# Optimization experiments

Hardware: AMD Instinct MI355X
Metric: run time of the kernel (lower is better)

## Reference

```python
import jax, jax.numpy as jnp
import numpy as np

B, T, I, H, SEQLEN = 16384, 60, 32, 128, 30


def setup_inputs() -> dict:
    key = jax.random.key(0)
    ks = jax.random.split(key, 8)
    s_ih = 1.0 / np.sqrt(H)
    return {
        "x": jax.random.normal(ks[0], (B, T, I), dtype=jnp.float32),
        "h": jax.random.normal(ks[1], (1, B, H), dtype=jnp.float32),
        # GRU params (PyTorch layout: gates [r, z, n] stacked along dim 0)
        "W_ih": jax.random.uniform(ks[2], (3 * H, I), minval=-s_ih, maxval=s_ih, dtype=jnp.float32),
        "W_hh": jax.random.uniform(ks[3], (3 * H, H), minval=-s_ih, maxval=s_ih, dtype=jnp.float32),
        "b_ih": jax.random.uniform(ks[4], (3 * H,), minval=-s_ih, maxval=s_ih, dtype=jnp.float32),
        "b_hh": jax.random.uniform(ks[5], (3 * H,), minval=-s_ih, maxval=s_ih, dtype=jnp.float32),
        # output projection: hidden -> n_inputs
        "W_out": jax.random.uniform(ks[6], (I, H), minval=-s_ih, maxval=s_ih, dtype=jnp.float32),
        "b_out": jax.random.uniform(ks[7], (I,), minval=-s_ih, maxval=s_ih, dtype=jnp.float32),
    }


def _gru_cell(x_t, h, W_ih, W_hh, b_ih, b_hh):
    # x_t: [B, I], h: [B, H]
    gi = x_t @ W_ih.T + b_ih          # [B, 3H]
    gh = h @ W_hh.T + b_hh            # [B, 3H]
    i_r, i_z, i_n = jnp.split(gi, 3, axis=-1)
    h_r, h_z, h_n = jnp.split(gh, 3, axis=-1)
    r = jax.nn.sigmoid(i_r + h_r)
    z = jax.nn.sigmoid(i_z + h_z)
    n = jnp.tanh(i_n + r * h_n)
    return (1.0 - z) * n + z * h


def reference(x, h, W_ih, W_hh, b_ih, b_hh, W_out, b_out):
    xout = x[:, SEQLEN:, :]            # [B, steps, I]
    steps = xout.shape[1]
    h0 = h[0]                          # single layer, unidirectional -> [B, H]
    x0 = xout[:, 0, :]                 # [B, I]

    def step(carry, _):
        x_t, h_t = carry
        h_new = _gru_cell(x_t, h_t, W_ih, W_hh, b_ih, b_hh)
        y = h_new @ W_out.T + b_out    # [B, I], fed back as next input
        return (y, h_new), y

    _, ys = jax.lax.scan(step, (x0, h0), None, length=steps)  # ys: [steps, B, I]
    return jnp.transpose(ys, (1, 0, 2))                        # [B, steps, I]
```

## Files before the change

kernel.cpp:

```cpp
#include <hip/hip_runtime.h>


#define NB    16384
#define TT    60
#define II    32
#define HH    128
#define NSTEP 30
#define SEQ0  30
#define BM    64
#define XBS   40
#define ROWB  256
#define BUFB  (BM * ROWB)

#define WS_WSTAR 0
#define WS_BSTAR (384 * 128)

#define S_RZ (-1.4426950408889634f)
#define S_N  ( 2.8853900817779268f)

typedef __attribute__((ext_vector_type(8))) short bf16x8;
typedef __attribute__((ext_vector_type(4))) float f32x4;

#define MFMA(a, b, c) __builtin_amdgcn_mfma_f32_16x16x32_bf16((a), (b), (c), 0, 0, 0)

#define LDS_BARRIER() do {                                          \
    asm volatile("s_waitcnt lgkmcnt(0)\n\ts_barrier" ::: "memory"); \
    __builtin_amdgcn_sched_barrier(0);                              \
} while (0)

#define EXP2(x) __builtin_amdgcn_exp2f(x)
#define RCP(x)  __builtin_amdgcn_rcpf(x)

__device__ __forceinline__ short f2bf(float x) {
    unsigned u = __float_as_uint(x);
    u += 0x7FFFu + ((u >> 16) & 1u);
    return (short)(u >> 16);
}
__device__ __forceinline__ unsigned cvt_pk_bf16(float lo, float hi) {
    unsigned r;
    asm("v_cvt_pk_bf16_f32 %0, %1, %2" : "=v"(r) : "v"(lo), "v"(hi));
    return r;
}
__device__ __forceinline__ bf16x8 ldw8(const float* p) {
    float4 a = *(const float4*)p;
    float4 b = *(const float4*)(p + 4);
    bf16x8 f;
    f[0] = f2bf(a.x); f[1] = f2bf(a.y); f[2] = f2bf(a.z); f[3] = f2bf(a.w);
    f[4] = f2bf(b.x); f[5] = f2bf(b.y); f[6] = f2bf(b.z); f[7] = f2bf(b.w);
    return f;
}
__device__ __forceinline__ bf16x8 ldw8s(const float* p, float s) {
    float4 a = *(const float4*)p;
    float4 b = *(const float4*)(p + 4);
    bf16x8 f;
    f[0] = f2bf(a.x * s); f[1] = f2bf(a.y * s); f[2] = f2bf(a.z * s); f[3] = f2bf(a.w * s);
    f[4] = f2bf(b.x * s); f[5] = f2bf(b.y * s); f[6] = f2bf(b.z * s); f[7] = f2bf(b.w * s);
    return f;
}
__device__ __forceinline__ float sigm2(float ap) { return RCP(1.0f + EXP2(ap)); }
__device__ __forceinline__ float tanh2(float tp) {
    return fmaf(-2.0f, RCP(1.0f + EXP2(tp)), 1.0f);
}

__global__ void fold_kernel(const float* __restrict__ Wih,
                            const float* __restrict__ Whh,
                            const float* __restrict__ bih,
                            const float* __restrict__ bhh,
                            const float* __restrict__ Wout,
                            const float* __restrict__ bout,
                            float* __restrict__ ws)
{
    const int jg = blockIdx.x;
    const int k  = threadIdx.x;
    const int gate = jg >> 7;
    const float sc = (gate < 2) ? S_RZ : S_N;
    float acc  = (gate < 2) ? Whh[(size_t)jg * HH + k] : 0.0f;
    float bacc = 0.0f;
    #pragma unroll 8
    for (int i = 0; i < II; ++i) {
        const float w = Wih[(size_t)jg * II + i];
        acc  += w * Wout[(size_t)i * HH + k];
        bacc += w * bout[i];
    }
    ws[WS_WSTAR + (size_t)jg * HH + k] = acc * sc;
    if (k == 0)
        ws[WS_BSTAR + jg] = (bih[jg] + ((gate < 2) ? bhh[jg] : 0.0f) + bacc) * sc;
}

__global__ __launch_bounds__(512, 1)
void gru_mfma_kernel(const float* __restrict__ x,
                     const float* __restrict__ h0,
                     const float* __restrict__ Wih,
                     const float* __restrict__ Whh,
                     const float* __restrict__ bih,
                     const float* __restrict__ bhh,
                     const float* __restrict__ Wout,
                     const float* __restrict__ bout,
                     const float* __restrict__ ws,
                     float* __restrict__ out)
{
    __shared__ short shb[2][BM * 128];
    __shared__ short sxb[BM * XBS];
    char* shbb = (char*)shb;

    const int tid    = threadIdx.x;
    const int lane   = tid & 63;
    const int wave   = __builtin_amdgcn_readfirstlane(tid >> 6);
    const int n16    = lane & 15;
    const int quad   = lane >> 4;
    const int rowblk = blockIdx.x * BM;
    const int j      = wave * 16 + n16;

    int rb[4];
    #pragma unroll
    for (int kt = 0; kt < 4; ++kt)
        rb[kt] = n16 * 256 + ((kt * 64 + quad * 16) ^ (n16 << 4));
    int wb[4];
    #pragma unroll
    for (int rg = 0; rg < 4; ++rg)
        wb[rg] = quad * 1024 + ((2 * j) ^ (quad << 6) ^ (rg << 4));

    bf16x8 Bnh[4];
    float  b_nh;
    {
        const float* wn = Whh + (size_t)(2 * HH + j) * HH;
        #pragma unroll
        for (int kt = 0; kt < 4; ++kt)
            Bnh[kt] = ldw8s(wn + kt * 32 + quad * 8, S_N);
        b_nh = bhh[2 * HH + j] * S_N;
    }
    const int rowtile = wave >> 1;
    const int coltile = wave & 1;
    bf16x8 Bo[4];
    float  b_o;
    {
        const int i = coltile * 16 + n16;
        #pragma unroll
        for (int kt = 0; kt < 4; ++kt)
            Bo[kt] = ldw8(Wout + (size_t)i * HH + kt * 32 + quad * 8);
        b_o = bout[i];
    }

    float hst[4][4];
    #pragma unroll
    for (int mt = 0; mt < 4; ++mt)
        #pragma unroll
        for (int reg = 0; reg < 4; ++reg)
            hst[mt][reg] = h0[(size_t)(rowblk + mt * 16 + quad * 4 + reg) * HH + j];

    float* yp0;
    float* yp1;
    {
        const int r0 = rowblk + rowtile * 16 + quad * 4;
        yp0 = out + (size_t)r0 * (NSTEP * II) + coltile * 16 + n16;
        yp1 = yp0 + 2 * (size_t)(NSTEP * II);
    }

    {
        const int r  = tid >> 3;
        const int cb = (tid & 7) * 32;
        const int sw = (r & 15) << 4;
        const float* src = h0 + (size_t)(rowblk + r) * HH + (tid & 7) * 16;
        *(bf16x8*)(shbb + r * ROWB + (cb ^ sw))        = ldw8(src);
        *(bf16x8*)(shbb + r * ROWB + ((cb + 16) ^ sw)) = ldw8(src + 8);
    }
    if (tid < 256) {
        const int r  = tid >> 2;
        const int c0 = (tid & 3) * 8;
        *(bf16x8*)&sxb[r * XBS + c0] = ldw8(x + ((size_t)(rowblk + r) * TT + SEQ0) * II + c0);
    }
    __syncthreads();

    {
        bf16x8 Br0[4], Bz0[4], Bxr, Bxz, Bxn;
        const float* wr = Whh + (size_t)j * HH;
        const float* wz = Whh + (size_t)(HH + j) * HH;
        #pragma unroll
        for (int kt = 0; kt < 4; ++kt) {
            Br0[kt] = ldw8s(wr + kt * 32 + quad * 8, S_RZ);
            Bz0[kt] = ldw8s(wz + kt * 32 + quad * 8, S_RZ);
        }
        Bxr = ldw8s(Wih + (size_t)j * II + quad * 8, S_RZ);
        Bxz = ldw8s(Wih + (size_t)(HH + j) * II + quad * 8, S_RZ);
        Bxn = ldw8s(Wih + (size_t)(2 * HH + j) * II + quad * 8, S_N);
        const float b_r0 = (bih[j] + bhh[j]) * S_RZ;
        const float b_z0 = (bih[HH + j] + bhh[HH + j]) * S_RZ;
        const float b_n0 = bih[2 * HH + j] * S_N;

        #pragma unroll
        for (int mt = 0; mt < 4; ++mt) {
            f32x4 ar  = (f32x4){b_r0, b_r0, b_r0, b_r0};
            f32x4 az  = (f32x4){b_z0, b_z0, b_z0, b_z0};
            f32x4 anh = (f32x4){b_nh, b_nh, b_nh, b_nh};
            f32x4 anx = (f32x4){b_n0, b_n0, b_n0, b_n0};
            #pragma unroll
            for (int kt = 0; kt < 4; ++kt) {
                bf16x8 A = *(const bf16x8*)(shbb + rb[kt] + mt * 4096);
                ar  = MFMA(A, Br0[kt], ar);
                az  = MFMA(A, Bz0[kt], az);
                anh = MFMA(A, Bnh[kt], anh);
            }
            {
                bf16x8 Ax = *(const bf16x8*)&sxb[(mt * 16 + n16) * XBS + quad * 8];
                ar  = MFMA(Ax, Bxr, ar);
                az  = MFMA(Ax, Bxz, az);
                anx = MFMA(Ax, Bxn, anx);
            }
            float hn[4];
            #pragma unroll
            for (int reg = 0; reg < 4; ++reg) {
                const float r = sigm2(ar[reg]);
                const float z = sigm2(az[reg]);
                const float n = tanh2(anx[reg] + r * anh[reg]);
                const float hnew = n + z * (hst[mt][reg] - n);
                hst[mt][reg] = hnew;
                hn[reg] = hnew;
            }
            const unsigned pk01 = cvt_pk_bf16(hn[0], hn[1]);
            const unsigned pk23 = cvt_pk_bf16(hn[2], hn[3]);
            *(short*)(shbb + BUFB + wb[0] + mt * 4096)       = (short)pk01;
            *(short*)(shbb + BUFB + wb[1] + mt * 4096 + 256) = (short)(pk01 >> 16);
            *(short*)(shbb + BUFB + wb[2] + mt * 4096 + 512) = (short)pk23;
            *(short*)(shbb + BUFB + wb[3] + mt * 4096 + 768) = (short)(pk23 >> 16);
        }
    }

    bf16x8 Brs[4], Bzs[4], Bni[4];
    float  b_rs, b_zs, b_ni;
    {
        const float* pr = ws + WS_WSTAR + (size_t)j * HH;
        const float* pz = ws + WS_WSTAR + (size_t)(HH + j) * HH;
        const float* pn = ws + WS_WSTAR + (size_t)(2 * HH + j) * HH;
        #pragma unroll
        for (int kt = 0; kt < 4; ++kt) {
            Brs[kt] = ldw8(pr + kt * 32 + quad * 8);
            Bzs[kt] = ldw8(pz + kt * 32 + quad * 8);
            Bni[kt] = ldw8(pn + kt * 32 + quad * 8);
        }
        b_rs = ws[WS_BSTAR + j];
        b_zs = ws[WS_BSTAR + HH + j];
        b_ni = ws[WS_BSTAR + 2 * HH + j];
    }

    __syncthreads();

    auto body = [&](int s, int qb, bool last) {
        (void)s;
        const int rdoff = qb * BUFB;
        {
            f32x4 yo = (f32x4){b_o, b_o, b_o, b_o};
            #pragma unroll
            for (int kt = 0; kt < 4; ++kt) {
                bf16x8 A2 = *(const bf16x8*)(shbb + rdoff + rb[kt] + rowtile * 4096);
                yo = MFMA(A2, Bo[kt], yo);
            }
            yp0[0]         = yo[0];
            yp0[NSTEP*II]  = yo[1];
            yp1[0]         = yo[2];
            yp1[NSTEP*II]  = yo[3];
            yp0 += II;
            yp1 += II;
        }
        if (last) return;

        const int wroff = (qb ^ 1) * BUFB;
        #pragma unroll
        for (int mt = 0; mt < 4; ++mt) {
            f32x4 ar  = (f32x4){b_rs, b_rs, b_rs, b_rs};
            f32x4 az  = (f32x4){b_zs, b_zs, b_zs, b_zs};
            f32x4 anh = (f32x4){b_nh, b_nh, b_nh, b_nh};
            f32x4 ani = (f32x4){b_ni, b_ni, b_ni, b_ni};
            #pragma unroll
            for (int kt = 0; kt < 4; ++kt) {
                bf16x8 A = *(const bf16x8*)(shbb + rdoff + rb[kt] + mt * 4096);
                ar  = MFMA(A, Brs[kt], ar);
                az  = MFMA(A, Bzs[kt], az);
                anh = MFMA(A, Bnh[kt], anh);
                ani = MFMA(A, Bni[kt], ani);
            }
            float hn[4];
            #pragma unroll
            for (int reg = 0; reg < 4; ++reg) {
                const float r = sigm2(ar[reg]);
                const float z = sigm2(az[reg]);
                const float n = tanh2(ani[reg] + r * anh[reg]);
                const float hnew = n + z * (hst[mt][reg] - n);
                hst[mt][reg] = hnew;
                hn[reg] = hnew;
            }
            const unsigned pk01 = cvt_pk_bf16(hn[0], hn[1]);
            const unsigned pk23 = cvt_pk_bf16(hn[2], hn[3]);
            *(short*)(shbb + wroff + wb[0] + mt * 4096)       = (short)pk01;
            *(short*)(shbb + wroff + wb[1] + mt * 4096 + 256) = (short)(pk01 >> 16);
            *(short*)(shbb + wroff + wb[2] + mt * 4096 + 512) = (short)pk23;
            *(short*)(shbb + wroff + wb[3] + mt * 4096 + 768) = (short)(pk23 >> 16);
        }
        LDS_BARRIER();
    };

    for (int s2 = 0; s2 < NSTEP - 2; s2 += 2) {
        body(s2,     1, false);
        body(s2 + 1, 0, false);
    }
    body(NSTEP - 2, 1, false);
    body(NSTEP - 1, 0, true);
}

extern "C" void kernel_launch(void* const* d_in, const int* in_sizes, int n_in,
                              void* d_out, int out_size, void* d_ws, size_t ws_size,
                              hipStream_t stream) {
    (void)in_sizes; (void)n_in; (void)out_size; (void)ws_size;
    const float* x    = (const float*)d_in[0];
    const float* h0   = (const float*)d_in[1];
    const float* Wih  = (const float*)d_in[2];
    const float* Whh  = (const float*)d_in[3];
    const float* bih  = (const float*)d_in[4];
    const float* bhh  = (const float*)d_in[5];
    const float* Wout = (const float*)d_in[6];
    const float* bout = (const float*)d_in[7];
    float* out = (float*)d_out;
    float* ws  = (float*)d_ws;

    fold_kernel<<<dim3(384), dim3(128), 0, stream>>>(Wih, Whh, bih, bhh,
                                                     Wout, bout, ws);
    dim3 grid(NB / BM);
    dim3 block(512);
    gru_mfma_kernel<<<grid, block, 0, stream>>>(x, h0, Wih, Whh, bih, bhh,
                                                Wout, bout, ws, out);
}
```

Baseline: 256.8 us.

## Split each 64-row block across 16 waves and stage W_out in LDS

Doubles the block to 1024 threads so each column-tile wave handles only half of the 64 rows, with two row-halves each covering 32 rows. This halves per-wave MFMA and gate work per step and the number of hidden-state registers held. The output projection weights move from per-wave registers into shared memory, and only the first 8 waves compute the output projection. The aim is more wave-level parallelism per CU to hide MFMA and transcendental latency in the serial recurrence. The cost is larger barriers, extra LDS reads for W_out, and uneven work between waves.

```diff
diff --git a/kernel.cpp b/kernel.cpp
--- a/kernel.cpp
+++ b/kernel.cpp
@@ -87,7 +87,7 @@
         ws[WS_BSTAR + jg] = (bih[jg] + ((gate < 2) ? bhh[jg] : 0.0f) + bacc) * sc;
 }
 
-__global__ __launch_bounds__(512, 1)
+__global__ __launch_bounds__(1024, 1)
 void gru_mfma_kernel(const float* __restrict__ x,
                      const float* __restrict__ h0,
                      const float* __restrict__ Wih,
@@ -101,6 +101,7 @@
 {
     __shared__ short shb[2][BM * 128];
     __shared__ short sxb[BM * XBS];
+    __shared__ short sWo[2 * 4 * 64 * 8];
     char* shbb = (char*)shb;
 
     const int tid    = threadIdx.x;
@@ -109,16 +110,24 @@
     const int n16    = lane & 15;
     const int quad   = lane >> 4;
     const int rowblk = blockIdx.x * BM;
-    const int j      = wave * 16 + n16;
+    const int ct     = wave & 7;
+    const int rh     = wave >> 3;
+    const int j      = ct * 16 + n16;
 
     int rb[4];
     #pragma unroll
     for (int kt = 0; kt < 4; ++kt)
-        rb[kt] = n16 * 256 + ((kt * 64 + quad * 16) ^ (n16 << 4));
+        rb[kt] = rh * 8192 + n16 * 256 + ((kt * 64 + quad * 16) ^ (n16 << 4));
     int wb[4];
     #pragma unroll
     for (int rg = 0; rg < 4; ++rg)
-        wb[rg] = quad * 1024 + ((2 * j) ^ (quad << 6) ^ (rg << 4));
+        wb[rg] = rh * 8192 + quad * 1024 + ((2 * j) ^ (quad << 6) ^ (rg << 4));
+    const int rowtile = (wave >> 1) & 3;
+    const int coltile = wave & 1;
+    int rb2[4];
+    #pragma unroll
+    for (int kt = 0; kt < 4; ++kt)
+        rb2[kt] = rowtile * 4096 + n16 * 256 + ((kt * 64 + quad * 16) ^ (n16 << 4));
 
     bf16x8 Bnh[4];
     float  b_nh;
@@ -129,24 +138,22 @@
             Bnh[kt] = ldw8s(wn + kt * 32 + quad * 8, S_N);
         b_nh = bhh[2 * HH + j] * S_N;
     }
-    const int rowtile = wave >> 1;
-    const int coltile = wave & 1;
-    bf16x8 Bo[4];
-    float  b_o;
-    {
-        const int i = coltile * 16 + n16;
-        #pragma unroll
-        for (int kt = 0; kt < 4; ++kt)
-            Bo[kt] = ldw8(Wout + (size_t)i * HH + kt * 32 + quad * 8);
-        b_o = bout[i];
-    }
-
-    float hst[4][4];
+    if (wave < 2) {
+        #pragma unroll
+        for (int kt = 0; kt < 4; ++kt) {
+            bf16x8 t = ldw8(Wout + (size_t)(wave * 16 + n16) * HH + kt * 32 + quad * 8);
+            *(bf16x8*)&sWo[((wave * 4 + kt) * 64 + lane) * 8] = t;
+        }
+    }
+    const float b_o = bout[coltile * 16 + n16];
+
+    float hst[2][4];
     #pragma unroll
-    for (int mt = 0; mt < 4; ++mt)
+    for (int mt = 0; mt < 2; ++mt)
         #pragma unroll
         for (int reg = 0; reg < 4; ++reg)
-            hst[mt][reg] = h0[(size_t)(rowblk + mt * 16 + quad * 4 + reg) * HH + j];
+            hst[mt][reg] =
+                h0[(size_t)(rowblk + rh * 32 + mt * 16 + quad * 4 + reg) * HH + j];
 
     float* yp0;
     float* yp1;
@@ -157,12 +164,11 @@
     }
 
     {
-        const int r  = tid >> 3;
-        const int cb = (tid & 7) * 32;
+        const int r  = tid >> 4;
+        const int cb = (tid & 15) * 16;
         const int sw = (r & 15) << 4;
-        const float* src = h0 + (size_t)(rowblk + r) * HH + (tid & 7) * 16;
-        *(bf16x8*)(shbb + r * ROWB + (cb ^ sw))        = ldw8(src);
-        *(bf16x8*)(shbb + r * ROWB + ((cb + 16) ^ sw)) = ldw8(src + 8);
+        *(bf16x8*)(shbb + r * ROWB + (cb ^ sw)) =
+            ldw8(h0 + (size_t)(rowblk + r) * HH + (tid & 15) * 8);
     }
     if (tid < 256) {
         const int r  = tid >> 2;
@@ -188,7 +194,7 @@
         const float b_n0 = bih[2 * HH + j] * S_N;
 
         #pragma unroll
-        for (int mt = 0; mt < 4; ++mt) {
+        for (int mt = 0; mt < 2; ++mt) {
             f32x4 ar  = (f32x4){b_r0, b_r0, b_r0, b_r0};
             f32x4 az  = (f32x4){b_z0, b_z0, b_z0, b_z0};
             f32x4 anh = (f32x4){b_nh, b_nh, b_nh, b_nh};
@@ -201,7 +207,7 @@
                 anh = MFMA(A, Bnh[kt], anh);
             }
             {
-                bf16x8 Ax = *(const bf16x8*)&sxb[(mt * 16 + n16) * XBS + quad * 8];
+                bf16x8 Ax = *(const bf16x8*)&sxb[(rh * 32 + mt * 16 + n16) * XBS + quad * 8];
                 ar  = MFMA(Ax, Bxr, ar);
                 az  = MFMA(Ax, Bxz, az);
                 anx = MFMA(Ax, Bxn, anx);
@@ -244,20 +250,20 @@
 
     __syncthreads();
 
-    auto body = [&](int s, int qb, bool last) {
-        (void)s;
+    auto body = [&](int qb, bool last) {
         const int rdoff = qb * BUFB;
-        {
+        if (wave < 8) {
             f32x4 yo = (f32x4){b_o, b_o, b_o, b_o};
             #pragma unroll
             for (int kt = 0; kt < 4; ++kt) {
-                bf16x8 A2 = *(const bf16x8*)(shbb + rdoff + rb[kt] + rowtile * 4096);
-                yo = MFMA(A2, Bo[kt], yo);
-            }
-            yp0[0]         = yo[0];
-            yp0[NSTEP*II]  = yo[1];
-            yp1[0]         = yo[2];
-            yp1[NSTEP*II]  = yo[3];
+                bf16x8 A2  = *(const bf16x8*)(shbb + rdoff + rb2[kt]);
+                bf16x8 Bof = *(const bf16x8*)&sWo[((coltile * 4 + kt) * 64 + lane) * 8];
+                yo = MFMA(A2, Bof, yo);
+            }
+            yp0[0]        = yo[0];
+            yp0[NSTEP*II] = yo[1];
+            yp1[0]        = yo[2];
+            yp1[NSTEP*II] = yo[3];
             yp0 += II;
             yp1 += II;
         }
@@ -265,7 +271,7 @@
 
         const int wroff = (qb ^ 1) * BUFB;
         #pragma unroll
-        for (int mt = 0; mt < 4; ++mt) {
+        for (int mt = 0; mt < 2; ++mt) {
             f32x4 ar  = (f32x4){b_rs, b_rs, b_rs, b_rs};
             f32x4 az  = (f32x4){b_zs, b_zs, b_zs, b_zs};
             f32x4 anh = (f32x4){b_nh, b_nh, b_nh, b_nh};
@@ -299,11 +305,11 @@
     };
 
     for (int s2 = 0; s2 < NSTEP - 2; s2 += 2) {
-        body(s2,     1, false);
-        body(s2 + 1, 0, false);
-    }
-    body(NSTEP - 2, 1, false);
-    body(NSTEP - 1, 0, true);
+        body(1, false);
+        body(0, false);
+    }
+    body(1, false);
+    body(0, true);
 }
 
 extern "C" void kernel_launch(void* const* d_in, const int* in_sizes, int n_in,
@@ -324,7 +330,7 @@
     fold_kernel<<<dim3(384), dim3(128), 0, stream>>>(Wih, Whh, bih, bhh,
                                                      Wout, bout, ws);
     dim3 grid(NB / BM);
-    dim3 block(512);
+    dim3 block(1024);
     gru_mfma_kernel<<<grid, block, 0, stream>>>(x, h0, Wih, Whh, bih, bhh,
                                                 Wout, bout, ws, out);
 }
```

After: 274.4 us. 1.07x slower.

## Software-pipeline GRU step so gate MFMAs overlap activations of previous tile

Applied to the files above, without the earlier changes.

Restructures each recurrent step so MFMA work for row tiles runs one or two tiles ahead of the sigmoid/tanh activation and LDS writeback of earlier tiles, with sched_barriers fixing the interleave. The output-projection global stores are also deferred until after some gate MFMAs are issued, so their latency is hidden. Bias vectors are hoisted into preformed f32x4 registers. This raises register pressure from holding up to three tiles of accumulators at once, which could cause spills at 512 threads.

```diff
diff --git a/kernel.cpp b/kernel.cpp
--- a/kernel.cpp
+++ b/kernel.cpp
@@ -27,6 +27,8 @@
     asm volatile("s_waitcnt lgkmcnt(0)\n\ts_barrier" ::: "memory"); \
     __builtin_amdgcn_sched_barrier(0);                              \
 } while (0)
+
+#define SB() __builtin_amdgcn_sched_barrier(0)
 
 #define EXP2(x) __builtin_amdgcn_exp2f(x)
 #define RCP(x)  __builtin_amdgcn_rcpf(x)
@@ -86,6 +88,40 @@
     if (k == 0)
         ws[WS_BSTAR + jg] = (bih[jg] + ((gate < 2) ? bhh[jg] : 0.0f) + bacc) * sc;
 }
+
+#define MT_MFMA(mt, ar, az, anh, ani, rdoff) do {                              \
+    bf16x8 A0_ = *(const bf16x8*)(shbb + (rdoff) + rb[0] + (mt) * 4096);       \
+    bf16x8 A1_ = *(const bf16x8*)(shbb + (rdoff) + rb[1] + (mt) * 4096);       \
+    bf16x8 A2_ = *(const bf16x8*)(shbb + (rdoff) + rb[2] + (mt) * 4096);       \
+    bf16x8 A3_ = *(const bf16x8*)(shbb + (rdoff) + rb[3] + (mt) * 4096);       \
+    ar  = MFMA(A0_, Brs[0], vb_r);  az  = MFMA(A0_, Bzs[0], vb_z);             \
+    anh = MFMA(A0_, Bnh[0], vb_nh); ani = MFMA(A0_, Bni[0], vb_ni);            \
+    ar  = MFMA(A1_, Brs[1], ar);    az  = MFMA(A1_, Bzs[1], az);               \
+    anh = MFMA(A1_, Bnh[1], anh);   ani = MFMA(A1_, Bni[1], ani);              \
+    ar  = MFMA(A2_, Brs[2], ar);    az  = MFMA(A2_, Bzs[2], az);               \
+    anh = MFMA(A2_, Bnh[2], anh);   ani = MFMA(A2_, Bni[2], ani);              \
+    ar  = MFMA(A3_, Brs[3], ar);    az  = MFMA(A3_, Bzs[3], az);               \
+    anh = MFMA(A3_, Bnh[3], anh);   ani = MFMA(A3_, Bni[3], ani);              \
+} while (0)
+
+#define ACT_MT(mt, ar, az, anh, ani, wroff) do {                               \
+    float hn_[4];                                                              \
+    _Pragma("unroll")                                                          \
+    for (int rg_ = 0; rg_ < 4; ++rg_) {                                        \
+        const float r_ = sigm2((ar)[rg_]);                                     \
+        const float z_ = sigm2((az)[rg_]);                                     \
+        const float n_ = tanh2((ani)[rg_] + r_ * (anh)[rg_]);                  \
+        const float h_ = n_ + z_ * (hst[mt][rg_] - n_);                        \
+        hst[mt][rg_] = h_;                                                     \
+        hn_[rg_] = h_;                                                         \
+    }                                                                          \
+    const unsigned pkA_ = cvt_pk_bf16(hn_[0], hn_[1]);                         \
+    const unsigned pkB_ = cvt_pk_bf16(hn_[2], hn_[3]);                         \
+    *(short*)(shbb + (wroff) + wb[0] + (mt) * 4096)       = (short)pkA_;       \
+    *(short*)(shbb + (wroff) + wb[1] + (mt) * 4096 + 256) = (short)(pkA_ >> 16); \
+    *(short*)(shbb + (wroff) + wb[2] + (mt) * 4096 + 512) = (short)pkB_;       \
+    *(short*)(shbb + (wroff) + wb[3] + (mt) * 4096 + 768) = (short)(pkB_ >> 16); \
+} while (0)
 
 __global__ __launch_bounds__(512, 1)
 void gru_mfma_kernel(const float* __restrict__ x,
@@ -226,7 +262,7 @@
     }
 
     bf16x8 Brs[4], Bzs[4], Bni[4];
-    float  b_rs, b_zs, b_ni;
+    f32x4  vb_r, vb_z, vb_nh, vb_ni, vb_o;
     {
         const float* pr = ws + WS_WSTAR + (size_t)j * HH;
         const float* pz = ws + WS_WSTAR + (size_t)(HH + j) * HH;
@@ -237,73 +273,73 @@
             Bzs[kt] = ldw8(pz + kt * 32 + quad * 8);
             Bni[kt] = ldw8(pn + kt * 32 + quad * 8);
         }
-        b_rs = ws[WS_BSTAR + j];
-        b_zs = ws[WS_BSTAR + HH + j];
-        b_ni = ws[WS_BSTAR + 2 * HH + j];
+        const float b_rs = ws[WS_BSTAR + j];
+        const float b_zs = ws[WS_BSTAR + HH + j];
+        const float b_ni = ws[WS_BSTAR + 2 * HH + j];
+        vb_r  = (f32x4){b_rs, b_rs, b_rs, b_rs};
+        vb_z  = (f32x4){b_zs, b_zs, b_zs, b_zs};
+        vb_nh = (f32x4){b_nh, b_nh, b_nh, b_nh};
+        vb_ni = (f32x4){b_ni, b_ni, b_ni, b_ni};
+        vb_o  = (f32x4){b_o,  b_o,  b_o,  b_o};
     }
 
     __syncthreads();
 
-    auto body = [&](int s, int qb, bool last) {
-        (void)s;
+    auto body = [&](int qb, bool last) {
         const int rdoff = qb * BUFB;
+        f32x4 yo;
         {
-            f32x4 yo = (f32x4){b_o, b_o, b_o, b_o};
-            #pragma unroll
-            for (int kt = 0; kt < 4; ++kt) {
-                bf16x8 A2 = *(const bf16x8*)(shbb + rdoff + rb[kt] + rowtile * 4096);
-                yo = MFMA(A2, Bo[kt], yo);
-            }
-            yp0[0]         = yo[0];
-            yp0[NSTEP*II]  = yo[1];
-            yp1[0]         = yo[2];
-            yp1[NSTEP*II]  = yo[3];
-            yp0 += II;
-            yp1 += II;
-        }
-        if (last) return;
-
+            bf16x8 Y0 = *(const bf16x8*)(shbb + rdoff + rb[0] + rowtile * 4096);
+            bf16x8 Y1 = *(const bf16x8*)(shbb + rdoff + rb[1] + rowtile * 4096);
+            bf16x8 Y2 = *(const bf16x8*)(shbb + rdoff + rb[2] + rowtile * 4096);
+            bf16x8 Y3 = *(const bf16x8*)(shbb + rdoff + rb[3] + rowtile * 4096);
+            yo = MFMA(Y0, Bo[0], vb_o);
+            yo = MFMA(Y1, Bo[1], yo);
+            yo = MFMA(Y2, Bo[2], yo);
+            yo = MFMA(Y3, Bo[3], yo);
+        }
+        if (last) {
+            yp0[0]        = yo[0];
+            yp0[NSTEP*II] = yo[1];
+            yp1[0]        = yo[2];
+            yp1[NSTEP*II] = yo[3];
+            return;
+        }
         const int wroff = (qb ^ 1) * BUFB;
-        #pragma unroll
-        for (int mt = 0; mt < 4; ++mt) {
-            f32x4 ar  = (f32x4){b_rs, b_rs, b_rs, b_rs};
-            f32x4 az  = (f32x4){b_zs, b_zs, b_zs, b_zs};
-            f32x4 anh = (f32x4){b_nh, b_nh, b_nh, b_nh};
-            f32x4 ani = (f32x4){b_ni, b_ni, b_ni, b_ni};
-            #pragma unroll
-            for (int kt = 0; kt < 4; ++kt) {
-                bf16x8 A = *(const bf16x8*)(shbb + rdoff + rb[kt] + mt * 4096);
-                ar  = MFMA(A, Brs[kt], ar);
-                az  = MFMA(A, Bzs[kt], az);
-                anh = MFMA(A, Bnh[kt], anh);
-                ani = MFMA(A, Bni[kt], ani);
-            }
-            float hn[4];
-            #pragma unroll
-            for (int reg = 0; reg < 4; ++reg) {
-                const float r = sigm2(ar[reg]);
-                const float z = sigm2(az[reg]);
-                const float n = tanh2(ani[reg] + r * anh[reg]);
-                const float hnew = n + z * (hst[mt][reg] - n);
-                hst[mt][reg] = hnew;
-                hn[reg] = hnew;
-            }
-            const unsigned pk01 = cvt_pk_bf16(hn[0], hn[1]);
-            const unsigned pk23 = cvt_pk_bf16(hn[2], hn[3]);
-            *(short*)(shbb + wroff + wb[0] + mt * 4096)       = (short)pk01;
-            *(short*)(shbb + wroff + wb[1] + mt * 4096 + 256) = (short)(pk01 >> 16);
-            *(short*)(shbb + wroff + wb[2] + mt * 4096 + 512) = (short)pk23;
-            *(short*)(shbb + wroff + wb[3] + mt * 4096 + 768) = (short)(pk23 >> 16);
-        }
+
+        f32x4 ar0, az0, anh0, ani0;
+        f32x4 ar1, az1, anh1, ani1;
+        MT_MFMA(0, ar0, az0, anh0, ani0, rdoff);
+        MT_MFMA(1, ar1, az1, anh1, ani1, rdoff);
+        SB();
+
+        f32x4 ar2, az2, anh2, ani2;
+        MT_MFMA(2, ar2, az2, anh2, ani2, rdoff);
+        yp0[0]        = yo[0];
+        yp0[NSTEP*II] = yo[1];
+        yp1[0]        = yo[2];
+        yp1[NSTEP*II] = yo[3];
+        yp0 += II;
+        yp1 += II;
+        ACT_MT(0, ar0, az0, anh0, ani0, wroff);
+        SB();
+
+        f32x4 ar3, az3, anh3, ani3;
+        MT_MFMA(3, ar3, az3, anh3, ani3, rdoff);
+        ACT_MT(1, ar1, az1, anh1, ani1, wroff);
+        SB();
+
+        ACT_MT(2, ar2, az2, anh2, ani2, wroff);
+        ACT_MT(3, ar3, az3, anh3, ani3, wroff);
         LDS_BARRIER();
     };
 
     for (int s2 = 0; s2 < NSTEP - 2; s2 += 2) {
-        body(s2,     1, false);
-        body(s2 + 1, 0, false);
-    }
-    body(NSTEP - 2, 1, false);
-    body(NSTEP - 1, 0, true);
+        body(1, false);
+        body(0, false);
+    }
+    body(1, false);
+    body(0, true);
 }
 
 extern "C" void kernel_launch(void* const* d_in, const int* in_sizes, int n_in,
```

Result: no change. 256.1 us (-0.3%).
